# Performance work log

Hardware: AMD Instinct MI355X
Metric: run time of the kernel (lower is better)

## Reference

```python
import jax, jax.numpy as jnp
import numpy as np

D_MODEL = 1024
NUM_HEADS = 16
HEAD_DIM = D_MODEL // NUM_HEADS
B, S = 4, 2048


def setup_inputs() -> dict:
    key = jax.random.key(0)
    ks = jax.random.split(key, 11)
    scale = 1.0 / np.sqrt(D_MODEL)
    return {
        "query": jax.random.normal(ks[0], (B, S, D_MODEL), jnp.float32),
        "key": jax.random.normal(ks[1], (B, S, D_MODEL), jnp.float32),
        "value": jax.random.normal(ks[2], (B, S, D_MODEL), jnp.float32),
        "Wq": jax.random.normal(ks[3], (D_MODEL, D_MODEL), jnp.float32) * scale,
        "bq": jnp.zeros((D_MODEL,), jnp.float32),
        "Wk": jax.random.normal(ks[4], (D_MODEL, D_MODEL), jnp.float32) * scale,
        "bk": jnp.zeros((D_MODEL,), jnp.float32),
        "Wv": jax.random.normal(ks[5], (D_MODEL, D_MODEL), jnp.float32) * scale,
        "bv": jnp.zeros((D_MODEL,), jnp.float32),
        "Wo": jax.random.normal(ks[6], (D_MODEL, D_MODEL), jnp.float32) * scale,
        "bo": jnp.zeros((D_MODEL,), jnp.float32),
    }


def reference(query, key, value, Wq, bq, Wk, bk, Wv, bv, Wo, bo):
    b = query.shape[0]
    # nn.Linear: x @ W.T + b; weights stored [out, in]
    def split_heads(x):
        return x.reshape(b, -1, NUM_HEADS, HEAD_DIM).transpose(0, 2, 1, 3)  # [b,h,s,d]
    q = split_heads(query @ Wq.T + bq)
    k = split_heads(key @ Wk.T + bk)
    v = split_heads(value @ Wv.T + bv)
    scores = jnp.einsum("bhqd,bhkd->bhqk", q, k) / np.sqrt(HEAD_DIM)
    weights = jax.nn.softmax(scores, axis=-1)
    out = jnp.einsum("bhqk,bhkd->bhqd", weights, v)
    out = out.transpose(0, 2, 1, 3).reshape(b, -1, D_MODEL)
    return out @ Wo.T + bo
```

## Files before the change

kernel.cpp:

```cpp
#include <hip/hip_runtime.h>

typedef __bf16 bf16;
typedef __bf16 bf16x8 __attribute__((ext_vector_type(8)));
typedef float f32x4 __attribute__((ext_vector_type(4)));

#define MFMA16(a, b, c) __builtin_amdgcn_mfma_f32_16x16x32_bf16((a), (b), (c), 0, 0, 0)

__device__ __forceinline__ void async_cp16(const bf16* g, bf16* l) {
    __builtin_amdgcn_global_load_lds((const __attribute__((address_space(1))) void*)g,
                                     (__attribute__((address_space(3))) void*)l, 16, 0, 0);
}

__global__ void cvt_bf16(const float* __restrict__ x, bf16* __restrict__ y, int n8) {
    int i = blockIdx.x * 256 + threadIdx.x;
    if (i >= n8) return;
    const float4* p = (const float4*)(x + (size_t)i * 8);
    float4 a = p[0], c = p[1];
    bf16x8 o;
    o[0] = (bf16)a.x; o[1] = (bf16)a.y; o[2] = (bf16)a.z; o[3] = (bf16)a.w;
    o[4] = (bf16)c.x; o[5] = (bf16)c.y; o[6] = (bf16)c.z; o[7] = (bf16)c.w;
    *(bf16x8*)(y + (size_t)i * 8) = o;
}

__global__ __launch_bounds__(256) void gemm_bt(
    const bf16* __restrict__ A, const bf16* __restrict__ W,
    const float* __restrict__ bias, void* __restrict__ Cout, int mode)
{
    __shared__ bf16 As[128 * 32];
    __shared__ bf16 Bs[128 * 32];
    const int K = 1024;
    const int tid = threadIdx.x;
    const int lane = tid & 63, wave = tid >> 6;
    const int l15 = lane & 15, quad = lane >> 4;
    const int wm = wave >> 1, wn = wave & 1;
    const int m0 = blockIdx.x * 128, n0 = blockIdx.y * 128;

    f32x4 acc[4][4] = {};

    const int r0 = tid >> 2, k8 = (tid & 3) * 8;
    const bf16* Ag0 = A + (size_t)(m0 + r0) * K + k8;
    const bf16* Ag1 = A + (size_t)(m0 + r0 + 64) * K + k8;
    const bf16* Wg0 = W + (size_t)(n0 + r0) * K + k8;
    const bf16* Wg1 = W + (size_t)(n0 + r0 + 64) * K + k8;
    bf16* Al0 = As + tid * 8;
    bf16* Al1 = As + (tid + 256) * 8;
    bf16* Bl0 = Bs + tid * 8;
    bf16* Bl1 = Bs + (tid + 256) * 8;

    for (int k0 = 0; k0 < K; k0 += 32) {
        __syncthreads();
        async_cp16(Ag0 + k0, Al0);
        async_cp16(Ag1 + k0, Al1);
        async_cp16(Wg0 + k0, Bl0);
        async_cp16(Wg1 + k0, Bl1);
        __syncthreads();

        bf16x8 af[4], bfr[4];
#pragma unroll
        for (int t = 0; t < 4; ++t) {
            af[t]  = *(const bf16x8*)(As + (wm * 64 + t * 16 + l15) * 32 + quad * 8);
            bfr[t] = *(const bf16x8*)(Bs + (wn * 64 + t * 16 + l15) * 32 + quad * 8);
        }
#pragma unroll
        for (int mt = 0; mt < 4; ++mt)
#pragma unroll
            for (int nt = 0; nt < 4; ++nt)
                acc[mt][nt] = MFMA16(af[mt], bfr[nt], acc[mt][nt]);
    }

#pragma unroll
    for (int mt = 0; mt < 4; ++mt) {
#pragma unroll
        for (int nt = 0; nt < 4; ++nt) {
            int col = n0 + wn * 64 + nt * 16 + l15;
            float bcol = (mode == 2) ? 0.0f : bias[col];
#pragma unroll
            for (int r = 0; r < 4; ++r) {
                int row = m0 + wm * 64 + mt * 16 + quad * 4 + r;
                float val = acc[mt][nt][r];
                if (mode == 2) {
                    val += bias[row];
                    int bb = col >> 11, s = col & 2047;
                    ((bf16*)Cout)[((size_t)(bb * 1024 + row) << 11) + s] = (bf16)val;
                } else if (mode == 3) {
                    ((float*)Cout)[(size_t)row * 1024 + col] = val + bcol;
                } else {
                    val += bcol;
                    if (mode == 0) val *= 0.125f;
                    int bb = row >> 11, s = row & 2047, hh = col >> 6, d = col & 63;
                    ((bf16*)Cout)[(((size_t)(bb * 16 + hh) * 2048 + s) << 6) + d] = (bf16)val;
                }
            }
        }
    }
}

__global__ __launch_bounds__(256, 2) void attn_kernel(
    const bf16* __restrict__ Qh, const bf16* __restrict__ Kh,
    const bf16* __restrict__ Vtg, bf16* __restrict__ AO)
{
    __shared__ bf16 Kl[64 * 72];
    __shared__ bf16 Vl[64 * 72];
    __shared__ bf16 Pl[4][64 * 72];

    const int tid = threadIdx.x;
    const int lane = tid & 63, wave = tid >> 6;
    const int l15 = lane & 15, quad = lane >> 4;
    const int h = blockIdx.y, b = blockIdx.z;
    const int bh = b * 16 + h;
    const size_t base = (size_t)bh << 17;
    const int q0 = blockIdx.x * 256 + wave * 64;

    bf16x8 qf[4][2];
#pragma unroll
    for (int mt = 0; mt < 4; ++mt)
#pragma unroll
        for (int ks = 0; ks < 2; ++ks)
            qf[mt][ks] = *(const bf16x8*)(Qh + base + (q0 + mt * 16 + l15) * 64 + ks * 32 + quad * 8);

    f32x4 o[4][4] = {};
    float ls[4][4] = {};

    const int rA = tid >> 3, sA = (tid & 7) * 8;
    const int rB = (tid + 256) >> 3, sB = sA;
    const bf16* Kg0 = Kh + base + rA * 64 + sA;
    const bf16* Kg1 = Kh + base + rB * 64 + sB;
    const bf16* Vg0 = Vtg + base + rA * 2048 + sA;
    const bf16* Vg1 = Vtg + base + rB * 2048 + sB;
    bf16* KlA = Kl + rA * 72 + sA;
    bf16* KlB = Kl + rB * 72 + sB;
    bf16* VlA = Vl + rA * 72 + sA;
    bf16* VlB = Vl + rB * 72 + sB;
    bf16* Pw = Pl[wave];

    bf16x8 kr0 = *(const bf16x8*)Kg0;
    bf16x8 kr1 = *(const bf16x8*)Kg1;
    bf16x8 vr0 = *(const bf16x8*)Vg0;
    bf16x8 vr1 = *(const bf16x8*)Vg1;

    for (int kt = 0; kt < 2048; kt += 64) {
        __syncthreads();
        *(bf16x8*)KlA = kr0;
        *(bf16x8*)KlB = kr1;
        *(bf16x8*)VlA = vr0;
        *(bf16x8*)VlB = vr1;
        __syncthreads();

        if (kt + 64 < 2048) {
            kr0 = *(const bf16x8*)(Kg0 + (kt + 64) * 64);
            kr1 = *(const bf16x8*)(Kg1 + (kt + 64) * 64);
            vr0 = *(const bf16x8*)(Vg0 + (kt + 64));
            vr1 = *(const bf16x8*)(Vg1 + (kt + 64));
        }

        bf16x8 kb[2][4];
#pragma unroll
        for (int ks = 0; ks < 2; ++ks)
#pragma unroll
            for (int nt = 0; nt < 4; ++nt)
                kb[ks][nt] = *(const bf16x8*)(Kl + (nt * 16 + l15) * 72 + ks * 32 + quad * 8);

#pragma unroll
        for (int mt = 0; mt < 4; ++mt) {
            f32x4 sc[4] = {};
#pragma unroll
            for (int ks = 0; ks < 2; ++ks)
#pragma unroll
                for (int nt = 0; nt < 4; ++nt)
                    sc[nt] = MFMA16(qf[mt][ks], kb[ks][nt], sc[nt]);
#pragma unroll
            for (int r = 0; r < 4; ++r) {
                int prow = (mt * 16 + quad * 4 + r) * 72;
                float sum = 0.0f;
#pragma unroll
                for (int nt = 0; nt < 4; ++nt) {
                    bf16 pb = (bf16)__expf(sc[nt][r]);
                    Pw[prow + nt * 16 + l15] = pb;
                    sum += (float)pb;
                }
                ls[mt][r] += sum;
            }
        }

        bf16x8 vb[2][4];
#pragma unroll
        for (int ks = 0; ks < 2; ++ks)
#pragma unroll
            for (int nt = 0; nt < 4; ++nt)
                vb[ks][nt] = *(const bf16x8*)(Vl + (nt * 16 + l15) * 72 + ks * 32 + quad * 8);
#pragma unroll
        for (int mt = 0; mt < 4; ++mt)
#pragma unroll
            for (int ks = 0; ks < 2; ++ks) {
                bf16x8 pa = *(const bf16x8*)(Pw + (mt * 16 + l15) * 72 + ks * 32 + quad * 8);
#pragma unroll
                for (int nt = 0; nt < 4; ++nt)
                    o[mt][nt] = MFMA16(pa, vb[ks][nt], o[mt][nt]);
            }
    }

#pragma unroll
    for (int mt = 0; mt < 4; ++mt)
#pragma unroll
        for (int r = 0; r < 4; ++r) {
            float l = ls[mt][r];
            l += __shfl_xor(l, 1, 64);
            l += __shfl_xor(l, 2, 64);
            l += __shfl_xor(l, 4, 64);
            l += __shfl_xor(l, 8, 64);
            float inv = 1.0f / l;
            int s = q0 + mt * 16 + quad * 4 + r;
            size_t rowbase = ((size_t)(b * 2048 + s)) * 1024 + h * 64;
#pragma unroll
            for (int nt = 0; nt < 4; ++nt)
                AO[rowbase + nt * 16 + l15] = (bf16)(o[mt][nt][r] * inv);
        }
}

extern "C" void kernel_launch(void* const* d_in, const int* in_sizes, int n_in,
                              void* d_out, int out_size, void* d_ws, size_t ws_size,
                              hipStream_t stream) {
    const float* q  = (const float*)d_in[0];
    const float* k  = (const float*)d_in[1];
    const float* v  = (const float*)d_in[2];
    const float* Wq = (const float*)d_in[3];
    const float* bq = (const float*)d_in[4];
    const float* Wk = (const float*)d_in[5];
    const float* bk = (const float*)d_in[6];
    const float* Wv = (const float*)d_in[7];
    const float* bv = (const float*)d_in[8];
    const float* Wo = (const float*)d_in[9];
    const float* bo = (const float*)d_in[10];
    float* out = (float*)d_out;

    const size_t NX = (size_t)8192 * 1024;
    const size_t NW = (size_t)1024 * 1024;
    bf16* ws  = (bf16*)d_ws;
    bf16* Xq  = ws;
    bf16* Xk  = Xq + NX;
    bf16* Xv  = Xk + NX;
    bf16* Wqb = Xv + NX;
    bf16* Wkb = Wqb + NW;
    bf16* Wvb = Wkb + NW;
    bf16* Wob = Wvb + NW;
    bf16* Qh  = Wob + NW;
    bf16* Kh  = Qh + NX;
    bf16* Vt  = Kh + NX;
    bf16* AO  = Xq;

    int nx8 = (int)(NX / 8), nw8 = (int)(NW / 8);
    cvt_bf16<<<nx8 / 256, 256, 0, stream>>>(q, Xq, nx8);
    cvt_bf16<<<nx8 / 256, 256, 0, stream>>>(k, Xk, nx8);
    cvt_bf16<<<nx8 / 256, 256, 0, stream>>>(v, Xv, nx8);
    cvt_bf16<<<nw8 / 256, 256, 0, stream>>>(Wq, Wqb, nw8);
    cvt_bf16<<<nw8 / 256, 256, 0, stream>>>(Wk, Wkb, nw8);
    cvt_bf16<<<nw8 / 256, 256, 0, stream>>>(Wv, Wvb, nw8);
    cvt_bf16<<<nw8 / 256, 256, 0, stream>>>(Wo, Wob, nw8);

    dim3 bb(256, 1, 1);
    gemm_bt<<<dim3(64, 8), bb, 0, stream>>>(Xq, Wqb, bq, Qh, 0);
    gemm_bt<<<dim3(64, 8), bb, 0, stream>>>(Xk, Wkb, bk, Kh, 1);
    gemm_bt<<<dim3(8, 64), bb, 0, stream>>>(Wvb, Xv, bv, Vt, 2);

    attn_kernel<<<dim3(8, 16, 4), bb, 0, stream>>>(Qh, Kh, Vt, AO);

    gemm_bt<<<dim3(64, 8), bb, 0, stream>>>(AO, Wob, bo, out, 3);
}
```

Baseline: 411.3 us.

## Batch QKV GEMMs into one launch, shrink attention tiles, use exp2

Merges the three QKV projection GEMMs into a single launch with a z-indexed argument struct, so 1536 blocks run together instead of three serial launches of 512. The attention kernel now gives each wave 32 query rows instead of 64, doubling the grid to 1024 blocks and raising occupancy to 4 blocks per CU, at the cost of loading K/V tiles twice as often per query. Softmax uses exp2 with log2(e) folded into the Q scale, and the row sum now accumulates unrounded fp32 values. Like the old code, softmax still subtracts no running max, relying on small scores.

```diff
diff --git a/kernel.cpp b/kernel.cpp
--- a/kernel.cpp
+++ b/kernel.cpp
@@ -5,6 +5,8 @@
 typedef float f32x4 __attribute__((ext_vector_type(4)));
 
 #define MFMA16(a, b, c) __builtin_amdgcn_mfma_f32_16x16x32_bf16((a), (b), (c), 0, 0, 0)
+
+#define QSCALE 0.1803368808f
 
 __device__ __forceinline__ void async_cp16(const bf16* g, bf16* l) {
     __builtin_amdgcn_global_load_lds((const __attribute__((address_space(1))) void*)g,
@@ -22,9 +24,10 @@
     *(bf16x8*)(y + (size_t)i * 8) = o;
 }
 
-__global__ __launch_bounds__(256) void gemm_bt(
+__device__ __forceinline__ void gemm_core(
     const bf16* __restrict__ A, const bf16* __restrict__ W,
-    const float* __restrict__ bias, void* __restrict__ Cout, int mode)
+    const float* __restrict__ bias, void* __restrict__ Cout,
+    int mode, int m0, int n0)
 {
     __shared__ bf16 As[128 * 32];
     __shared__ bf16 Bs[128 * 32];
@@ -33,7 +36,6 @@
     const int lane = tid & 63, wave = tid >> 6;
     const int l15 = lane & 15, quad = lane >> 4;
     const int wm = wave >> 1, wn = wave & 1;
-    const int m0 = blockIdx.x * 128, n0 = blockIdx.y * 128;
 
     f32x4 acc[4][4] = {};
 
@@ -86,7 +88,7 @@
                     ((float*)Cout)[(size_t)row * 1024 + col] = val + bcol;
                 } else {
                     val += bcol;
-                    if (mode == 0) val *= 0.125f;
+                    if (mode == 0) val *= QSCALE;
                     int bb = row >> 11, s = row & 2047, hh = col >> 6, d = col & 63;
                     ((bf16*)Cout)[(((size_t)(bb * 16 + hh) * 2048 + s) << 6) + d] = (bf16)val;
                 }
@@ -95,13 +97,35 @@
     }
 }
 
-__global__ __launch_bounds__(256, 2) void attn_kernel(
+struct QkvArgs {
+    const bf16* A[3];
+    const bf16* W[3];
+    const float* bias[3];
+    bf16* out[3];
+};
+
+__global__ __launch_bounds__(256) void qkv_gemm(QkvArgs t) {
+    int z = blockIdx.y;
+    int bx = blockIdx.x;
+    int m0, n0;
+    if (z < 2) { m0 = (bx & 63) * 128; n0 = (bx >> 6) * 128; }
+    else       { m0 = (bx & 7) * 128;  n0 = (bx >> 3) * 128; }
+    gemm_core(t.A[z], t.W[z], t.bias[z], t.out[z], z, m0, n0);
+}
+
+__global__ __launch_bounds__(256) void oproj_gemm(
+    const bf16* __restrict__ A, const bf16* __restrict__ W,
+    const float* __restrict__ bias, float* __restrict__ Cout) {
+    gemm_core(A, W, bias, Cout, 3, blockIdx.x * 128, blockIdx.y * 128);
+}
+
+__global__ __launch_bounds__(256, 4) void attn_kernel(
     const bf16* __restrict__ Qh, const bf16* __restrict__ Kh,
     const bf16* __restrict__ Vtg, bf16* __restrict__ AO)
 {
     __shared__ bf16 Kl[64 * 72];
     __shared__ bf16 Vl[64 * 72];
-    __shared__ bf16 Pl[4][64 * 72];
+    __shared__ bf16 Pl[4][32 * 72];
 
     const int tid = threadIdx.x;
     const int lane = tid & 63, wave = tid >> 6;
@@ -109,28 +133,28 @@
     const int h = blockIdx.y, b = blockIdx.z;
     const int bh = b * 16 + h;
     const size_t base = (size_t)bh << 17;
-    const int q0 = blockIdx.x * 256 + wave * 64;
-
-    bf16x8 qf[4][2];
-#pragma unroll
-    for (int mt = 0; mt < 4; ++mt)
+    const int q0 = blockIdx.x * 128 + wave * 32;
+
+    bf16x8 qf[2][2];
+#pragma unroll
+    for (int mt = 0; mt < 2; ++mt)
 #pragma unroll
         for (int ks = 0; ks < 2; ++ks)
             qf[mt][ks] = *(const bf16x8*)(Qh + base + (q0 + mt * 16 + l15) * 64 + ks * 32 + quad * 8);
 
-    f32x4 o[4][4] = {};
-    float ls[4][4] = {};
+    f32x4 o[2][4] = {};
+    float ls[2][4] = {};
 
     const int rA = tid >> 3, sA = (tid & 7) * 8;
-    const int rB = (tid + 256) >> 3, sB = sA;
+    const int rB = rA + 32;
     const bf16* Kg0 = Kh + base + rA * 64 + sA;
-    const bf16* Kg1 = Kh + base + rB * 64 + sB;
+    const bf16* Kg1 = Kh + base + rB * 64 + sA;
     const bf16* Vg0 = Vtg + base + rA * 2048 + sA;
-    const bf16* Vg1 = Vtg + base + rB * 2048 + sB;
+    const bf16* Vg1 = Vtg + base + rB * 2048 + sA;
     bf16* KlA = Kl + rA * 72 + sA;
-    bf16* KlB = Kl + rB * 72 + sB;
+    bf16* KlB = Kl + rB * 72 + sA;
     bf16* VlA = Vl + rA * 72 + sA;
-    bf16* VlB = Vl + rB * 72 + sB;
+    bf16* VlB = Vl + rB * 72 + sA;
     bf16* Pw = Pl[wave];
 
     bf16x8 kr0 = *(const bf16x8*)Kg0;
@@ -161,7 +185,7 @@
                 kb[ks][nt] = *(const bf16x8*)(Kl + (nt * 16 + l15) * 72 + ks * 32 + quad * 8);
 
 #pragma unroll
-        for (int mt = 0; mt < 4; ++mt) {
+        for (int mt = 0; mt < 2; ++mt) {
             f32x4 sc[4] = {};
 #pragma unroll
             for (int ks = 0; ks < 2; ++ks)
@@ -174,9 +198,9 @@
                 float sum = 0.0f;
 #pragma unroll
                 for (int nt = 0; nt < 4; ++nt) {
-                    bf16 pb = (bf16)__expf(sc[nt][r]);
-                    Pw[prow + nt * 16 + l15] = pb;
-                    sum += (float)pb;
+                    float pf = __builtin_amdgcn_exp2f(sc[nt][r]);
+                    Pw[prow + nt * 16 + l15] = (bf16)pf;
+                    sum += pf;
                 }
                 ls[mt][r] += sum;
             }
@@ -189,7 +213,7 @@
             for (int nt = 0; nt < 4; ++nt)
                 vb[ks][nt] = *(const bf16x8*)(Vl + (nt * 16 + l15) * 72 + ks * 32 + quad * 8);
 #pragma unroll
-        for (int mt = 0; mt < 4; ++mt)
+        for (int mt = 0; mt < 2; ++mt)
 #pragma unroll
             for (int ks = 0; ks < 2; ++ks) {
                 bf16x8 pa = *(const bf16x8*)(Pw + (mt * 16 + l15) * 72 + ks * 32 + quad * 8);
@@ -200,7 +224,7 @@
     }
 
 #pragma unroll
-    for (int mt = 0; mt < 4; ++mt)
+    for (int mt = 0; mt < 2; ++mt)
 #pragma unroll
         for (int r = 0; r < 4; ++r) {
             float l = ls[mt][r];
@@ -258,11 +282,13 @@
     cvt_bf16<<<nw8 / 256, 256, 0, stream>>>(Wo, Wob, nw8);
 
     dim3 bb(256, 1, 1);
-    gemm_bt<<<dim3(64, 8), bb, 0, stream>>>(Xq, Wqb, bq, Qh, 0);
-    gemm_bt<<<dim3(64, 8), bb, 0, stream>>>(Xk, Wkb, bk, Kh, 1);
-    gemm_bt<<<dim3(8, 64), bb, 0, stream>>>(Wvb, Xv, bv, Vt, 2);
-
-    attn_kernel<<<dim3(8, 16, 4), bb, 0, stream>>>(Qh, Kh, Vt, AO);
-
-    gemm_bt<<<dim3(64, 8), bb, 0, stream>>>(AO, Wob, bo, out, 3);
-}
+    QkvArgs t;
+    t.A[0] = Xq;  t.W[0] = Wqb; t.bias[0] = bq; t.out[0] = Qh;
+    t.A[1] = Xk;  t.W[1] = Wkb; t.bias[1] = bk; t.out[1] = Kh;
+    t.A[2] = Wvb; t.W[2] = Xv;  t.bias[2] = bv; t.out[2] = Vt;
+    qkv_gemm<<<dim3(512, 3), bb, 0, stream>>>(t);
+
+    attn_kernel<<<dim3(16, 16, 4), bb, 0, stream>>>(Qh, Kh, Vt, AO);
+
+    oproj_gemm<<<dim3(64, 8), bb, 0, stream>>>(AO, Wob, bo, out);
+}
```

New measurement: 414.3 us. Within noise of the previous version (+0.7%).
